# Kernel optimization log

Measured on AMD Instinct MI355X. Metric: run time of the kernel, lower is better.

The kernel has to match this reference:

```python
import jax, jax.numpy as jnp
import numpy as np


def setup_inputs() -> dict:
    key = jax.random.key(0)
    k1, k2, k3 = jax.random.split(key, 3)
    B, Lx, Ly, D = 8, 2048, 2048, 512  # D = 2*hidden_size
    x = jax.random.normal(k1, (B, Lx, D), dtype=jnp.float32)
    y = jax.random.normal(k2, (B, Ly, D), dtype=jnp.float32)
    # torch nn.Linear weight: [out_features, in_features], applied as x @ W.T
    Wb = jax.random.normal(k3, (D, D), dtype=jnp.float32) * (1.0 / np.sqrt(D))
    return {"x": x, "y": y, "Wb": Wb}


def reference(x, y, Wb):
    # _s1 = Wb(x).transpose(2,1): project x then transpose -> scores s_jt = y @ (x Wb^T)^T
    xw = jnp.einsum('bxd,ed->bxe', x, Wb)          # [B, Lx, D], equals x @ Wb.T
    sjt = jnp.einsum('byd,bxd->byx', y, xw)        # [B, Ly, Lx]
    ait = jax.nn.softmax(sjt, axis=-1)             # softmax over Lx
    qtb = jnp.einsum('byx,bxd->byd', ait, x)       # [B, Ly, D]
    return qtb
```

## Files before the change

kernel.cpp:

```cpp
#include <hip/hip_runtime.h>
#include <hip/hip_bf16.h>
#include <math.h>

#define D_DIM 512
#define LX 2048
#define LY 2048
#define NB 8

typedef float f32x4 __attribute__((ext_vector_type(4)));
typedef __bf16 bf16x8 __attribute__((ext_vector_type(8)));

__device__ __forceinline__ unsigned short f2bf_rn(float f) {
    unsigned u = __float_as_uint(f);
    unsigned r = (u + 0x7fffu + ((u >> 16) & 1u)) >> 16;
    return (unsigned short)r;
}
__device__ __forceinline__ float bf2f(unsigned short h) {
    return __uint_as_float(((unsigned)h) << 16);
}
__device__ __forceinline__ void async16(void* lds, const void* g) {
    __builtin_amdgcn_global_load_lds(
        (const __attribute__((address_space(1))) void*)g,
        (__attribute__((address_space(3))) void*)lds, 16, 0, 0);
}
__device__ __forceinline__ bf16x8 ldfrag(const char* p) {
    return *(const bf16x8*)p;
}

__global__ __launch_bounds__(256) void prep_k(
    const float* __restrict__ x, const float* __restrict__ y,
    const float* __restrict__ Wb,
    unsigned short* __restrict__ xfh, unsigned short* __restrict__ xfl,
    unsigned short* __restrict__ yfh, unsigned short* __restrict__ yfl,
    unsigned short* __restrict__ wfh, unsigned short* __restrict__ wfl,
    unsigned short* __restrict__ xtf)
{
    __shared__ unsigned short T2[64][72];
    const int blk = blockIdx.x, tid = threadIdx.x;

    if (blk < 8320) {
        const float* src; unsigned short *dh, *dl; int base;
        if (blk < 4096)      { src = x;  dh = xfh; dl = xfl; base = blk; }
        else if (blk < 8192) { src = y;  dh = yfh; dl = yfl; base = blk - 4096; }
        else                 { src = Wb; dh = wfh; dl = wfl; base = blk - 8192; }
        int fbid = base * 4 + (tid >> 6);
        int lane = tid & 63;
        int r16 = fbid >> 4, k32 = fbid & 15;
        int row = r16 * 16 + (lane & 15);
        int col = k32 * 32 + (lane >> 4) * 8;
        const float* s = src + (size_t)row * D_DIM + col;
        float4 v0 = *(const float4*)s;
        float4 v1 = *(const float4*)(s + 4);
        float vv[8] = {v0.x, v0.y, v0.z, v0.w, v1.x, v1.y, v1.z, v1.w};
        unsigned hh[4], ll[4];
        #pragma unroll
        for (int k = 0; k < 4; ++k) {
            unsigned short ha = f2bf_rn(vv[2*k]),   hb = f2bf_rn(vv[2*k+1]);
            unsigned short la = f2bf_rn(vv[2*k]   - bf2f(ha));
            unsigned short lb = f2bf_rn(vv[2*k+1] - bf2f(hb));
            hh[k] = (unsigned)ha | ((unsigned)hb << 16);
            ll[k] = (unsigned)la | ((unsigned)lb << 16);
        }
        size_t off = (size_t)fbid * 512 + lane * 8;
        *(uint4*)(dh + off) = make_uint4(hh[0], hh[1], hh[2], hh[3]);
        *(uint4*)(dl + off) = make_uint4(ll[0], ll[1], ll[2], ll[3]);
    } else {
        int idx = blk - 8320;
        int ct = idx & 31, dt = (idx >> 5) & 7, b = idx >> 8;
        const float* xb = x + (size_t)b * LX * D_DIM;
        int rc = tid >> 4;
        int d4 = (tid & 15) * 4;
        #pragma unroll
        for (int i = 0; i < 4; ++i) {
            int cl = rc + i * 16;
            float4 v = *(const float4*)(xb + (size_t)(ct * 64 + cl) * D_DIM + dt * 64 + d4);
            T2[d4 + 0][cl] = f2bf_rn(v.x);
            T2[d4 + 1][cl] = f2bf_rn(v.y);
            T2[d4 + 2][cl] = f2bf_rn(v.z);
            T2[d4 + 3][cl] = f2bf_rn(v.w);
        }
        __syncthreads();
        #pragma unroll
        for (int si = 0; si < 2; ++si) {
            int s = tid + si * 256;
            int fb = s >> 6, lane = s & 63;
            int dd16l = fb >> 1, c32l = fb & 1;
            int ddl = dd16l * 16 + (lane & 15);
            int cl  = c32l * 32 + (lane >> 4) * 8;
            uint4 v = *(const uint4*)&T2[ddl][cl];
            size_t off = ((size_t)((b * 32 + dt * 4 + dd16l) * 64 + (ct * 2 + c32l)) * 64 + lane) * 8;
            *(uint4*)(xtf + off) = v;
        }
    }
}

__global__ __launch_bounds__(256, 2) void xw_mfma_k(
    const unsigned short* __restrict__ xfh, const unsigned short* __restrict__ xfl,
    const unsigned short* __restrict__ wfh, const unsigned short* __restrict__ wfl,
    unsigned short* __restrict__ xwfh, unsigned short* __restrict__ xwfl)
{
    __shared__ char smem[49152];
    const int tid = threadIdx.x, lane = tid & 63, w = tid >> 6;
    const int Mt = blockIdx.x, Nt = blockIdx.y;

    f32x4 acc[2][4];
    #pragma unroll
    for (int m = 0; m < 2; ++m)
        #pragma unroll
        for (int n = 0; n < 4; ++n) acc[m][n] = (f32x4){0.f, 0.f, 0.f, 0.f};

    auto stage = [&](int kc, int buf) {
        char* sb = smem + buf * 24576;
        #pragma unroll
        for (int i = 0; i < 4; ++i) {
            int s = w + 4 * i;
            int c16l = s >> 1, h = s & 1;
            size_t fb = ((size_t)(Mt * 8 + c16l)) * 16 + kc;
            const unsigned short* src = (h ? xfl : xfh) + fb * 512 + lane * 8;
            async16(sb + h * 8192 + c16l * 1024 + lane * 16, src);
        }
        #pragma unroll
        for (int i = 0; i < 2; ++i) {
            int s = w + 4 * i;
            int n16l = s >> 1, h = s & 1;
            size_t fb = ((size_t)(Nt * 4 + n16l)) * 16 + kc;
            const unsigned short* src = (h ? wfl : wfh) + fb * 512 + lane * 8;
            async16(sb + 16384 + h * 4096 + n16l * 1024 + lane * 16, src);
        }
    };

    stage(0, 0);
    __syncthreads();
    for (int kc = 0; kc < 16; ++kc) {
        if (kc < 15) stage(kc + 1, (kc + 1) & 1);
        char* sb = smem + (kc & 1) * 24576;
        bf16x8 ah[2], al[2], bh[4], bl[4];
        #pragma unroll
        for (int m = 0; m < 2; ++m) {
            int c16l = w * 2 + m;
            ah[m] = ldfrag(sb + c16l * 1024 + lane * 16);
            al[m] = ldfrag(sb + 8192 + c16l * 1024 + lane * 16);
        }
        #pragma unroll
        for (int n = 0; n < 4; ++n) {
            bh[n] = ldfrag(sb + 16384 + n * 1024 + lane * 16);
            bl[n] = ldfrag(sb + 20480 + n * 1024 + lane * 16);
        }
        #pragma unroll
        for (int m = 0; m < 2; ++m)
            #pragma unroll
            for (int n = 0; n < 4; ++n) {
                acc[m][n] = __builtin_amdgcn_mfma_f32_16x16x32_bf16(ah[m], bh[n], acc[m][n], 0, 0, 0);
                acc[m][n] = __builtin_amdgcn_mfma_f32_16x16x32_bf16(ah[m], bl[n], acc[m][n], 0, 0, 0);
                acc[m][n] = __builtin_amdgcn_mfma_f32_16x16x32_bf16(al[m], bh[n], acc[m][n], 0, 0, 0);
            }
        __syncthreads();
    }

    float* E = (float*)smem;
    const int q = lane >> 4, c15 = lane & 15;
    #pragma unroll
    for (int m = 0; m < 2; ++m)
        #pragma unroll
        for (int n = 0; n < 4; ++n)
            #pragma unroll
            for (int r = 0; r < 4; ++r)
                E[(w * 32 + m * 16 + q * 4 + r) * 68 + n * 16 + c15] = acc[m][n][r];
    __syncthreads();
    #pragma unroll
    for (int i = 0; i < 4; ++i) {
        int s = tid + i * 256;
        int c16l = s >> 7, e32l = (s >> 6) & 1, lp = s & 63;
        int row = c16l * 16 + (lp & 15), col = e32l * 32 + (lp >> 4) * 8;
        const float* sp = E + row * 68 + col;
        unsigned hh[4], ll[4];
        #pragma unroll
        for (int k = 0; k < 4; ++k) {
            float a = sp[2 * k], bq = sp[2 * k + 1];
            unsigned short ha = f2bf_rn(a), hb = f2bf_rn(bq);
            unsigned short la = f2bf_rn(a - bf2f(ha)), lb = f2bf_rn(bq - bf2f(hb));
            hh[k] = (unsigned)ha | ((unsigned)hb << 16);
            ll[k] = (unsigned)la | ((unsigned)lb << 16);
        }
        size_t fb = (size_t)(Mt * 8 + c16l) * 16 + (Nt * 2 + e32l);
        *(uint4*)(xwfh + fb * 512 + lp * 8) = make_uint4(hh[0], hh[1], hh[2], hh[3]);
        *(uint4*)(xwfl + fb * 512 + lp * 8) = make_uint4(ll[0], ll[1], ll[2], ll[3]);
    }
}

#define SBUF_STRIDE 20480

__global__ __launch_bounds__(256, 2) void flash3_k(
    const unsigned short* __restrict__ yfh, const unsigned short* __restrict__ yfl,
    const unsigned short* __restrict__ xwfh, const unsigned short* __restrict__ xwfl,
    const unsigned short* __restrict__ xtf, float* __restrict__ out)
{
    __shared__ char smem[74752];
    const int tid = threadIdx.x, lane = tid & 63, w = tid >> 6;
    const int jt = blockIdx.x, b = blockIdx.y;
    const int q = lane >> 4, c15 = lane & 15;
    unsigned short* Pf = (unsigned short*)(smem + 65536);
    float* red_max = (float*)(smem + 73728);
    float* red_sum = (float*)(smem + 74240);

    f32x4 o[2][8];
    #pragma unroll
    for (int m = 0; m < 2; ++m)
        #pragma unroll
        for (int n = 0; n < 8; ++n) o[m][n] = (f32x4){0.f, 0.f, 0.f, 0.f};
    float m_run[2][4], l_run[2][4];
    #pragma unroll
    for (int m = 0; m < 2; ++m)
        #pragma unroll
        for (int r = 0; r < 4; ++r) { m_run[m][r] = -INFINITY; l_run[m][r] = 0.f; }

    auto stage_s = [&](int xt, int kc, int buf) {
        char* sb = smem + buf * SBUF_STRIDE;
        #pragma unroll
        for (int i = 0; i < 4; ++i) {
            int s = w + 4 * i;
            int c16l = s >> 1, h = s & 1;
            size_t fb = ((size_t)(b * 128 + xt * 8 + c16l)) * 16 + kc;
            const unsigned short* src = (h ? xwfl : xwfh) + fb * 512 + lane * 8;
            async16(sb + h * 8192 + c16l * 1024 + lane * 16, src);
        }
        {
            int j16l = w & 1, h = w >> 1;
            size_t fb = ((size_t)(b * 128 + jt * 2 + j16l)) * 16 + kc;
            const unsigned short* src = (h ? yfl : yfh) + fb * 512 + lane * 8;
            async16(sb + 16384 + h * 2048 + j16l * 1024 + lane * 16, src);
        }
    };
    auto stage_x = [&](int xt, int cc, int buf) {
        char* xb = smem + buf * 32768;
        #pragma unroll
        for (int i = 0; i < 8; ++i) {
            int dd16 = w + 4 * i;
            size_t off = (((size_t)(b * 32 + dd16)) * 64 + (xt * 4 + cc)) * 512 + lane * 8;
            async16(xb + dd16 * 1024 + lane * 16, xtf + off);
        }
    };

    for (int xt = 0; xt < 16; ++xt) {
        f32x4 sa[2][2];
        #pragma unroll
        for (int m = 0; m < 2; ++m)
            #pragma unroll
            for (int n = 0; n < 2; ++n) sa[m][n] = (f32x4){0.f, 0.f, 0.f, 0.f};

        stage_s(xt, 0, 0);
        __syncthreads();
        for (int kc = 0; kc < 16; ++kc) {
            if (kc < 15) stage_s(xt, kc + 1, (kc + 1) & 1);
            char* sb = smem + (kc & 1) * SBUF_STRIDE;
            bf16x8 ah[2], al[2];
            ah[0] = ldfrag(sb + 16384 + lane * 16);
            ah[1] = ldfrag(sb + 17408 + lane * 16);
            al[0] = ldfrag(sb + 18432 + lane * 16);
            al[1] = ldfrag(sb + 19456 + lane * 16);
            #pragma unroll
            for (int n = 0; n < 2; ++n) {
                int c16l = w * 2 + n;
                bf16x8 bh = ldfrag(sb + c16l * 1024 + lane * 16);
                bf16x8 bl = ldfrag(sb + 8192 + c16l * 1024 + lane * 16);
                #pragma unroll
                for (int m = 0; m < 2; ++m) {
                    sa[m][n] = __builtin_amdgcn_mfma_f32_16x16x32_bf16(ah[m], bh, sa[m][n], 0, 0, 0);
                    sa[m][n] = __builtin_amdgcn_mfma_f32_16x16x32_bf16(ah[m], bl, sa[m][n], 0, 0, 0);
                    sa[m][n] = __builtin_amdgcn_mfma_f32_16x16x32_bf16(al[m], bh, sa[m][n], 0, 0, 0);
                }
            }
            __syncthreads();
        }

        float pmax[2][4];
        #pragma unroll
        for (int m = 0; m < 2; ++m)
            #pragma unroll
            for (int r = 0; r < 4; ++r) pmax[m][r] = fmaxf(sa[m][0][r], sa[m][1][r]);
        #pragma unroll
        for (int d = 1; d < 16; d <<= 1)
            #pragma unroll
            for (int m = 0; m < 2; ++m)
                #pragma unroll
                for (int r = 0; r < 4; ++r)
                    pmax[m][r] = fmaxf(pmax[m][r], __shfl_xor(pmax[m][r], d, 64));
        if (c15 == 0) {
            #pragma unroll
            for (int m = 0; m < 2; ++m)
                #pragma unroll
                for (int r = 0; r < 4; ++r)
                    red_max[w * 32 + m * 16 + q * 4 + r] = pmax[m][r];
        }
        __syncthreads();
        float mnew[2][4], alpha[2][4];
        #pragma unroll
        for (int m = 0; m < 2; ++m)
            #pragma unroll
            for (int r = 0; r < 4; ++r) {
                int j = m * 16 + q * 4 + r;
                float t = fmaxf(fmaxf(red_max[j], red_max[32 + j]),
                                fmaxf(red_max[64 + j], red_max[96 + j]));
                float mn = fmaxf(m_run[m][r], t);
                mnew[m][r] = mn;
                alpha[m][r] = __expf(m_run[m][r] - mn);
                m_run[m][r] = mn;
            }
        float psum[2][4] = {};
        #pragma unroll
        for (int m = 0; m < 2; ++m)
            #pragma unroll
            for (int n = 0; n < 2; ++n)
                #pragma unroll
                for (int r = 0; r < 4; ++r) {
                    float p = __expf(sa[m][n][r] - mnew[m][r]);
                    sa[m][n][r] = p;
                    psum[m][r] += (n == 0) ? p - psum[m][r] * 0.f : p;
                }
        #pragma unroll
        for (int d = 1; d < 16; d <<= 1)
            #pragma unroll
            for (int m = 0; m < 2; ++m)
                #pragma unroll
                for (int r = 0; r < 4; ++r)
                    psum[m][r] += __shfl_xor(psum[m][r], d, 64);
        if (c15 == 0) {
            #pragma unroll
            for (int m = 0; m < 2; ++m)
                #pragma unroll
                for (int r = 0; r < 4; ++r)
                    red_sum[w * 32 + m * 16 + q * 4 + r] = psum[m][r];
        }
        #pragma unroll
        for (int m = 0; m < 2; ++m)
            #pragma unroll
            for (int n = 0; n < 2; ++n)
                #pragma unroll
                for (int r = 0; r < 4; ++r) {
                    int cl = n * 16 + c15;
                    int lp = (q * 4 + r) + 16 * (cl >> 3);
                    Pf[((m * 4 + w) * 64 + lp) * 8 + (cl & 7)] = f2bf_rn(sa[m][n][r]);
                }
        __syncthreads();
        #pragma unroll
        for (int m = 0; m < 2; ++m)
            #pragma unroll
            for (int r = 0; r < 4; ++r) {
                int j = m * 16 + q * 4 + r;
                float ts = red_sum[j] + red_sum[32 + j] + red_sum[64 + j] + red_sum[96 + j];
                l_run[m][r] = l_run[m][r] * alpha[m][r] + ts;
            }
        #pragma unroll
        for (int m = 0; m < 2; ++m)
            #pragma unroll
            for (int n = 0; n < 8; ++n)
                #pragma unroll
                for (int r = 0; r < 4; ++r) o[m][n][r] *= alpha[m][r];

        stage_x(xt, 0, 0);
        __syncthreads();
        for (int cc = 0; cc < 4; ++cc) {
            if (cc < 3) stage_x(xt, cc + 1, (cc + 1) & 1);
            char* xb = smem + (cc & 1) * 32768;
            bf16x8 pa0 = ldfrag((const char*)Pf + ((0 * 4 + cc) * 64 + lane) * 16);
            bf16x8 pa1 = ldfrag((const char*)Pf + ((1 * 4 + cc) * 64 + lane) * 16);
            #pragma unroll
            for (int n = 0; n < 8; ++n) {
                bf16x8 xv = ldfrag(xb + (w * 8 + n) * 1024 + lane * 16);
                o[0][n] = __builtin_amdgcn_mfma_f32_16x16x32_bf16(pa0, xv, o[0][n], 0, 0, 0);
                o[1][n] = __builtin_amdgcn_mfma_f32_16x16x32_bf16(pa1, xv, o[1][n], 0, 0, 0);
            }
            __syncthreads();
        }
    }

    #pragma unroll
    for (int m = 0; m < 2; ++m)
        #pragma unroll
        for (int r = 0; r < 4; ++r) {
            float inv = 1.0f / l_run[m][r];
            int j = jt * 32 + m * 16 + q * 4 + r;
            #pragma unroll
            for (int n = 0; n < 8; ++n) {
                int dd = w * 128 + n * 16 + c15;
                out[((size_t)(b * 2048 + j)) * 512 + dd] = o[m][n][r] * inv;
            }
        }
}

__global__ __launch_bounds__(256) void xw_gemm_fb(
    const float* __restrict__ x, const float* __restrict__ Wb, float* __restrict__ xw)
{
    __shared__ float As[16][68];
    __shared__ float Bs[16][68];
    const int tid = threadIdx.x;
    const int bm = blockIdx.x * 64, bn = blockIdx.y * 64;
    const int tm = (tid & 15) * 4, tn = (tid >> 4) * 4;
    const int lrow = tid >> 2, lk = (tid & 3) * 4;
    const float* ag = x  + (size_t)(bm + lrow) * D_DIM + lk;
    const float* bg = Wb + (size_t)(bn + lrow) * D_DIM + lk;
    float acc[4][4] = {};
    for (int kt = 0; kt < D_DIM; kt += 16) {
        const float4 av = *(const float4*)(ag + kt);
        const float4 bv = *(const float4*)(bg + kt);
        __syncthreads();
        As[lk+0][lrow] = av.x; As[lk+1][lrow] = av.y; As[lk+2][lrow] = av.z; As[lk+3][lrow] = av.w;
        Bs[lk+0][lrow] = bv.x; Bs[lk+1][lrow] = bv.y; Bs[lk+2][lrow] = bv.z; Bs[lk+3][lrow] = bv.w;
        __syncthreads();
        #pragma unroll
        for (int k = 0; k < 16; ++k) {
            const float4 a = *(const float4*)&As[k][tm];
            const float4 bq = *(const float4*)&Bs[k][tn];
            const float* ap = (const float*)&a;
            const float* bp = (const float*)&bq;
            #pragma unroll
            for (int i = 0; i < 4; ++i)
                #pragma unroll
                for (int jj = 0; jj < 4; ++jj)
                    acc[i][jj] = fmaf(ap[i], bp[jj], acc[i][jj]);
        }
    }
    #pragma unroll
    for (int i = 0; i < 4; ++i)
        *(float4*)&xw[(size_t)(bm + tm + i) * D_DIM + bn + tn] =
            make_float4(acc[i][0], acc[i][1], acc[i][2], acc[i][3]);
}

__global__ __launch_bounds__(256) void flash_fb(
    const float* __restrict__ x, const float* __restrict__ y,
    const float* __restrict__ xw, float* __restrict__ out)
{
    __shared__ float Yl[16][516];
    __shared__ float XWl[64][68];
    __shared__ float Pl[16][68];
    __shared__ float Xl[8][512];
    const int tid = threadIdx.x, b = blockIdx.y, jtb = blockIdx.x;
    const int j = tid >> 4, tc = tid & 15, c0 = tc * 4;
    {
        const float* yg = y + (size_t)(b * LY + jtb * 16 + j) * D_DIM;
        #pragma unroll
        for (int ii = 0; ii < 8; ++ii)
            *(float4*)&Yl[j][tc * 4 + 64 * ii] = *(const float4*)(yg + tc * 4 + 64 * ii);
    }
    float4 o[8];
    #pragma unroll
    for (int ii = 0; ii < 8; ++ii) o[ii] = make_float4(0.f, 0.f, 0.f, 0.f);
    float m = -INFINITY, l = 0.f;
    const size_t xbase = (size_t)b * LX * D_DIM;
    for (int xtt = 0; xtt < LX / 64; ++xtt) {
        float sa[4] = {0.f, 0.f, 0.f, 0.f};
        for (int kcc = 0; kcc < D_DIM; kcc += 64) {
            const int sc = tid >> 2, skq = (tid & 3) * 4;
            const float* xwg = xw + xbase + (size_t)(xtt * 64 + sc) * D_DIM + kcc + skq;
            const float4 t0 = *(const float4*)(xwg + 0);
            const float4 t1 = *(const float4*)(xwg + 16);
            const float4 t2 = *(const float4*)(xwg + 32);
            const float4 t3 = *(const float4*)(xwg + 48);
            __syncthreads();
            XWl[skq+ 0][sc]=t0.x; XWl[skq+ 1][sc]=t0.y; XWl[skq+ 2][sc]=t0.z; XWl[skq+ 3][sc]=t0.w;
            XWl[skq+16][sc]=t1.x; XWl[skq+17][sc]=t1.y; XWl[skq+18][sc]=t1.z; XWl[skq+19][sc]=t1.w;
            XWl[skq+32][sc]=t2.x; XWl[skq+33][sc]=t2.y; XWl[skq+34][sc]=t2.z; XWl[skq+35][sc]=t2.w;
            XWl[skq+48][sc]=t3.x; XWl[skq+49][sc]=t3.y; XWl[skq+50][sc]=t3.z; XWl[skq+51][sc]=t3.w;
            __syncthreads();
            #pragma unroll
            for (int k4 = 0; k4 < 16; ++k4) {
                const float4 yv = *(const float4*)&Yl[j][kcc + k4 * 4];
                const float* yp = (const float*)&yv;
                #pragma unroll
                for (int ss = 0; ss < 4; ++ss) {
                    const float4 xv = *(const float4*)&XWl[k4 * 4 + ss][c0];
                    sa[0] = fmaf(yp[ss], xv.x, sa[0]);
                    sa[1] = fmaf(yp[ss], xv.y, sa[1]);
                    sa[2] = fmaf(yp[ss], xv.z, sa[2]);
                    sa[3] = fmaf(yp[ss], xv.w, sa[3]);
                }
            }
        }
        float tmax = fmaxf(fmaxf(sa[0], sa[1]), fmaxf(sa[2], sa[3]));
        #pragma unroll
        for (int ww = 1; ww < 16; ww <<= 1) tmax = fmaxf(tmax, __shfl_xor(tmax, ww, 64));
        const float mnew = fmaxf(m, tmax);
        const float scale = __expf(m - mnew);
        const float p0 = __expf(sa[0] - mnew), p1 = __expf(sa[1] - mnew);
        const float p2 = __expf(sa[2] - mnew), p3 = __expf(sa[3] - mnew);
        float ts = p0 + p1 + p2 + p3;
        #pragma unroll
        for (int ww = 1; ww < 16; ww <<= 1) ts += __shfl_xor(ts, ww, 64);
        l = l * scale + ts; m = mnew;
        #pragma unroll
        for (int ii = 0; ii < 8; ++ii) {
            o[ii].x *= scale; o[ii].y *= scale; o[ii].z *= scale; o[ii].w *= scale;
        }
        *(float4*)&Pl[j][c0] = make_float4(p0, p1, p2, p3);
        for (int ccc = 0; ccc < 8; ++ccc) {
            const int xr = tid >> 5, xq = (tid & 31) * 4;
            const float* xg = x + xbase + (size_t)(xtt * 64 + ccc * 8 + xr) * D_DIM + xq;
            const float4 x0 = *(const float4*)(xg + 0);
            const float4 x1 = *(const float4*)(xg + 128);
            const float4 x2 = *(const float4*)(xg + 256);
            const float4 x3 = *(const float4*)(xg + 384);
            __syncthreads();
            *(float4*)&Xl[xr][xq +   0] = x0; *(float4*)&Xl[xr][xq + 128] = x1;
            *(float4*)&Xl[xr][xq + 256] = x2; *(float4*)&Xl[xr][xq + 384] = x3;
            __syncthreads();
            #pragma unroll
            for (int c = 0; c < 8; ++c) {
                const float pv = Pl[j][ccc * 8 + c];
                #pragma unroll
                for (int ii = 0; ii < 8; ++ii) {
                    const float4 xv = *(const float4*)&Xl[c][tc * 4 + 64 * ii];
                    o[ii].x = fmaf(pv, xv.x, o[ii].x); o[ii].y = fmaf(pv, xv.y, o[ii].y);
                    o[ii].z = fmaf(pv, xv.z, o[ii].z); o[ii].w = fmaf(pv, xv.w, o[ii].w);
                }
            }
        }
    }
    const float inv = 1.0f / l;
    float* og = out + (size_t)(b * LY + jtb * 16 + j) * D_DIM;
    #pragma unroll
    for (int ii = 0; ii < 8; ++ii) {
        float4 v = o[ii];
        v.x *= inv; v.y *= inv; v.z *= inv; v.w *= inv;
        *(float4*)(og + tc * 4 + 64 * ii) = v;
    }
}

extern "C" void kernel_launch(void* const* d_in, const int* in_sizes, int n_in,
                              void* d_out, int out_size, void* d_ws, size_t ws_size,
                              hipStream_t stream)
{
    const float* x  = (const float*)d_in[0];
    const float* y  = (const float*)d_in[1];
    const float* Wb = (const float*)d_in[2];
    float* out = (float*)d_out;

    const size_t OFF_XFH = 0,         OFF_XFL = 16777216;
    const size_t OFF_YFH = 33554432,  OFF_YFL = 50331648;
    const size_t OFF_XTF = 67108864;
    const size_t OFF_XWH = 83886080,  OFF_XWL = 100663296;
    const size_t OFF_WFH = 117440512, OFF_WFL = 117964800;
    const size_t NEEDED  = 118489088;

    if (ws_size >= NEEDED) {
        char* ws = (char*)d_ws;
        unsigned short* xfh = (unsigned short*)(ws + OFF_XFH);
        unsigned short* xfl = (unsigned short*)(ws + OFF_XFL);
        unsigned short* yfh = (unsigned short*)(ws + OFF_YFH);
        unsigned short* yfl = (unsigned short*)(ws + OFF_YFL);
        unsigned short* xtf = (unsigned short*)(ws + OFF_XTF);
        unsigned short* xwfh = (unsigned short*)(ws + OFF_XWH);
        unsigned short* xwfl = (unsigned short*)(ws + OFF_XWL);
        unsigned short* wfh = (unsigned short*)(ws + OFF_WFH);
        unsigned short* wfl = (unsigned short*)(ws + OFF_WFL);

        prep_k<<<10368, 256, 0, stream>>>(x, y, Wb, xfh, xfl, yfh, yfl, wfh, wfl, xtf);
        dim3 g1(128, 8);
        xw_mfma_k<<<g1, 256, 0, stream>>>(xfh, xfl, wfh, wfl, xwfh, xwfl);
        dim3 g2(64, 8);
        flash3_k<<<g2, 256, 0, stream>>>(yfh, yfl, xwfh, xwfl, xtf, out);
    } else {
        float* xw = (float*)d_ws;
        dim3 g1(NB * LX / 64, D_DIM / 64);
        xw_gemm_fb<<<g1, 256, 0, stream>>>(x, Wb, xw);
        dim3 g2(LY / 16, NB);
        flash_fb<<<g2, 256, 0, stream>>>(x, y, xw, out);
    }
}
```

Before: 383.6 us.

## Double flash tile to 64 rows x 256 cols with 512-thread blocks

The attention kernel now uses 8 waves per block, split into 2 row halves by 4 column groups. Each block covers 64 query rows and 256 x positions per outer step, so there are half as many outer iterations and blocks. This is meant to raise operand reuse in shared memory and cut global reloads of the x and xW tiles per query row. It also issues the first x-tile prefetch before the softmax math to overlap that load with the exponentials. The cost is more LDS (about 114 KB) and twice as many score accumulators per wave, which may limit the kernel to one block per CU.

```diff
diff --git a/kernel.cpp b/kernel.cpp
--- a/kernel.cpp
+++ b/kernel.cpp
@@ -188,20 +188,22 @@
     }
 }
 
-#define SBUF_STRIDE 20480
-
-__global__ __launch_bounds__(256, 2) void flash3_k(
+#define SBUF 40960
+
+__global__ __launch_bounds__(512, 2) void flash4_k(
     const unsigned short* __restrict__ yfh, const unsigned short* __restrict__ yfl,
     const unsigned short* __restrict__ xwfh, const unsigned short* __restrict__ xwfl,
     const unsigned short* __restrict__ xtf, float* __restrict__ out)
 {
-    __shared__ char smem[74752];
+    __shared__ char smem[116736];
     const int tid = threadIdx.x, lane = tid & 63, w = tid >> 6;
     const int jt = blockIdx.x, b = blockIdx.y;
     const int q = lane >> 4, c15 = lane & 15;
-    unsigned short* Pf = (unsigned short*)(smem + 65536);
-    float* red_max = (float*)(smem + 73728);
-    float* red_sum = (float*)(smem + 74240);
+    const int jh = w >> 2;
+    const int cw = w & 3;
+    unsigned short* Pf = (unsigned short*)(smem + 81920);
+    float* red_max = (float*)(smem + 114688);
+    float* red_sum = (float*)(smem + 115712);
 
     f32x4 o[2][8];
     #pragma unroll
@@ -215,54 +217,55 @@
         for (int r = 0; r < 4; ++r) { m_run[m][r] = -INFINITY; l_run[m][r] = 0.f; }
 
     auto stage_s = [&](int xt, int kc, int buf) {
-        char* sb = smem + buf * SBUF_STRIDE;
+        char* sb = smem + buf * SBUF;
         #pragma unroll
         for (int i = 0; i < 4; ++i) {
-            int s = w + 4 * i;
+            int s = w + 8 * i;
             int c16l = s >> 1, h = s & 1;
-            size_t fb = ((size_t)(b * 128 + xt * 8 + c16l)) * 16 + kc;
+            size_t fb = ((size_t)(b * 128 + xt * 16 + c16l)) * 16 + kc;
             const unsigned short* src = (h ? xwfl : xwfh) + fb * 512 + lane * 8;
-            async16(sb + h * 8192 + c16l * 1024 + lane * 16, src);
+            async16(sb + h * 16384 + c16l * 1024 + lane * 16, src);
         }
         {
-            int j16l = w & 1, h = w >> 1;
-            size_t fb = ((size_t)(b * 128 + jt * 2 + j16l)) * 16 + kc;
+            int j16l = w & 3, h = w >> 2;
+            size_t fb = ((size_t)(b * 128 + jt * 4 + j16l)) * 16 + kc;
             const unsigned short* src = (h ? yfl : yfh) + fb * 512 + lane * 8;
-            async16(sb + 16384 + h * 2048 + j16l * 1024 + lane * 16, src);
+            async16(sb + 32768 + h * 4096 + j16l * 1024 + lane * 16, src);
         }
     };
     auto stage_x = [&](int xt, int cc, int buf) {
-        char* xb = smem + buf * 32768;
-        #pragma unroll
-        for (int i = 0; i < 8; ++i) {
-            int dd16 = w + 4 * i;
-            size_t off = (((size_t)(b * 32 + dd16)) * 64 + (xt * 4 + cc)) * 512 + lane * 8;
+        char* xb = smem + buf * SBUF;
+        #pragma unroll
+        for (int i = 0; i < 4; ++i) {
+            int dd16 = w + 8 * i;
+            size_t off = (((size_t)(b * 32 + dd16)) * 64 + (xt * 8 + cc)) * 512 + lane * 8;
             async16(xb + dd16 * 1024 + lane * 16, xtf + off);
         }
     };
 
-    for (int xt = 0; xt < 16; ++xt) {
-        f32x4 sa[2][2];
-        #pragma unroll
-        for (int m = 0; m < 2; ++m)
-            #pragma unroll
-            for (int n = 0; n < 2; ++n) sa[m][n] = (f32x4){0.f, 0.f, 0.f, 0.f};
+    for (int xt = 0; xt < 8; ++xt) {
+        f32x4 sa[2][4];
+        #pragma unroll
+        for (int m = 0; m < 2; ++m)
+            #pragma unroll
+            for (int n = 0; n < 4; ++n) sa[m][n] = (f32x4){0.f, 0.f, 0.f, 0.f};
 
         stage_s(xt, 0, 0);
         __syncthreads();
         for (int kc = 0; kc < 16; ++kc) {
             if (kc < 15) stage_s(xt, kc + 1, (kc + 1) & 1);
-            char* sb = smem + (kc & 1) * SBUF_STRIDE;
+            char* sb = smem + (kc & 1) * SBUF;
             bf16x8 ah[2], al[2];
-            ah[0] = ldfrag(sb + 16384 + lane * 16);
-            ah[1] = ldfrag(sb + 17408 + lane * 16);
-            al[0] = ldfrag(sb + 18432 + lane * 16);
-            al[1] = ldfrag(sb + 19456 + lane * 16);
-            #pragma unroll
-            for (int n = 0; n < 2; ++n) {
-                int c16l = w * 2 + n;
+            #pragma unroll
+            for (int m = 0; m < 2; ++m) {
+                ah[m] = ldfrag(sb + 32768 + (jh * 2 + m) * 1024 + lane * 16);
+                al[m] = ldfrag(sb + 36864 + (jh * 2 + m) * 1024 + lane * 16);
+            }
+            #pragma unroll
+            for (int n = 0; n < 4; ++n) {
+                int c16l = cw * 4 + n;
                 bf16x8 bh = ldfrag(sb + c16l * 1024 + lane * 16);
-                bf16x8 bl = ldfrag(sb + 8192 + c16l * 1024 + lane * 16);
+                bf16x8 bl = ldfrag(sb + 16384 + c16l * 1024 + lane * 16);
                 #pragma unroll
                 for (int m = 0; m < 2; ++m) {
                     sa[m][n] = __builtin_amdgcn_mfma_f32_16x16x32_bf16(ah[m], bh, sa[m][n], 0, 0, 0);
@@ -277,7 +280,9 @@
         #pragma unroll
         for (int m = 0; m < 2; ++m)
             #pragma unroll
-            for (int r = 0; r < 4; ++r) pmax[m][r] = fmaxf(sa[m][0][r], sa[m][1][r]);
+            for (int r = 0; r < 4; ++r)
+                pmax[m][r] = fmaxf(fmaxf(sa[m][0][r], sa[m][1][r]),
+                                   fmaxf(sa[m][2][r], sa[m][3][r]));
         #pragma unroll
         for (int d = 1; d < 16; d <<= 1)
             #pragma unroll
@@ -290,17 +295,18 @@
             for (int m = 0; m < 2; ++m)
                 #pragma unroll
                 for (int r = 0; r < 4; ++r)
-                    red_max[w * 32 + m * 16 + q * 4 + r] = pmax[m][r];
-        }
-        __syncthreads();
+                    red_max[cw * 64 + jh * 32 + m * 16 + q * 4 + r] = pmax[m][r];
+        }
+        __syncthreads();
+        stage_x(xt, 0, 0);
         float mnew[2][4], alpha[2][4];
         #pragma unroll
         for (int m = 0; m < 2; ++m)
             #pragma unroll
             for (int r = 0; r < 4; ++r) {
-                int j = m * 16 + q * 4 + r;
-                float t = fmaxf(fmaxf(red_max[j], red_max[32 + j]),
-                                fmaxf(red_max[64 + j], red_max[96 + j]));
+                int j = jh * 32 + m * 16 + q * 4 + r;
+                float t = fmaxf(fmaxf(red_max[j], red_max[64 + j]),
+                                fmaxf(red_max[128 + j], red_max[192 + j]));
                 float mn = fmaxf(m_run[m][r], t);
                 mnew[m][r] = mn;
                 alpha[m][r] = __expf(m_run[m][r] - mn);
@@ -310,12 +316,12 @@
         #pragma unroll
         for (int m = 0; m < 2; ++m)
             #pragma unroll
-            for (int n = 0; n < 2; ++n)
+            for (int n = 0; n < 4; ++n)
                 #pragma unroll
                 for (int r = 0; r < 4; ++r) {
                     float p = __expf(sa[m][n][r] - mnew[m][r]);
                     sa[m][n][r] = p;
-                    psum[m][r] += (n == 0) ? p - psum[m][r] * 0.f : p;
+                    psum[m][r] += p;
                 }
         #pragma unroll
         for (int d = 1; d < 16; d <<= 1)
@@ -329,25 +335,25 @@
             for (int m = 0; m < 2; ++m)
                 #pragma unroll
                 for (int r = 0; r < 4; ++r)
-                    red_sum[w * 32 + m * 16 + q * 4 + r] = psum[m][r];
-        }
-        #pragma unroll
-        for (int m = 0; m < 2; ++m)
-            #pragma unroll
-            for (int n = 0; n < 2; ++n)
+                    red_sum[cw * 64 + jh * 32 + m * 16 + q * 4 + r] = psum[m][r];
+        }
+        #pragma unroll
+        for (int m = 0; m < 2; ++m)
+            #pragma unroll
+            for (int n = 0; n < 4; ++n)
                 #pragma unroll
                 for (int r = 0; r < 4; ++r) {
-                    int cl = n * 16 + c15;
-                    int lp = (q * 4 + r) + 16 * (cl >> 3);
-                    Pf[((m * 4 + w) * 64 + lp) * 8 + (cl & 7)] = f2bf_rn(sa[m][n][r]);
+                    int blkP = (jh * 2 + m) * 8 + cw * 2 + (n >> 1);
+                    int lp = (q * 4 + r) + 16 * ((n & 1) * 2 + (c15 >> 3));
+                    Pf[(blkP * 64 + lp) * 8 + (c15 & 7)] = f2bf_rn(sa[m][n][r]);
                 }
         __syncthreads();
         #pragma unroll
         for (int m = 0; m < 2; ++m)
             #pragma unroll
             for (int r = 0; r < 4; ++r) {
-                int j = m * 16 + q * 4 + r;
-                float ts = red_sum[j] + red_sum[32 + j] + red_sum[64 + j] + red_sum[96 + j];
+                int j = jh * 32 + m * 16 + q * 4 + r;
+                float ts = red_sum[j] + red_sum[64 + j] + red_sum[128 + j] + red_sum[192 + j];
                 l_run[m][r] = l_run[m][r] * alpha[m][r] + ts;
             }
         #pragma unroll
@@ -357,16 +363,14 @@
                 #pragma unroll
                 for (int r = 0; r < 4; ++r) o[m][n][r] *= alpha[m][r];
 
-        stage_x(xt, 0, 0);
-        __syncthreads();
-        for (int cc = 0; cc < 4; ++cc) {
-            if (cc < 3) stage_x(xt, cc + 1, (cc + 1) & 1);
-            char* xb = smem + (cc & 1) * 32768;
-            bf16x8 pa0 = ldfrag((const char*)Pf + ((0 * 4 + cc) * 64 + lane) * 16);
-            bf16x8 pa1 = ldfrag((const char*)Pf + ((1 * 4 + cc) * 64 + lane) * 16);
+        for (int cc = 0; cc < 8; ++cc) {
+            if (cc < 7) stage_x(xt, cc + 1, (cc + 1) & 1);
+            char* xb = smem + (cc & 1) * SBUF;
+            bf16x8 pa0 = ldfrag((const char*)Pf + (((jh * 2 + 0) * 8 + cc) * 64 + lane) * 16);
+            bf16x8 pa1 = ldfrag((const char*)Pf + (((jh * 2 + 1) * 8 + cc) * 64 + lane) * 16);
             #pragma unroll
             for (int n = 0; n < 8; ++n) {
-                bf16x8 xv = ldfrag(xb + (w * 8 + n) * 1024 + lane * 16);
+                bf16x8 xv = ldfrag(xb + (cw * 8 + n) * 1024 + lane * 16);
                 o[0][n] = __builtin_amdgcn_mfma_f32_16x16x32_bf16(pa0, xv, o[0][n], 0, 0, 0);
                 o[1][n] = __builtin_amdgcn_mfma_f32_16x16x32_bf16(pa1, xv, o[1][n], 0, 0, 0);
             }
@@ -379,10 +383,10 @@
         #pragma unroll
         for (int r = 0; r < 4; ++r) {
             float inv = 1.0f / l_run[m][r];
-            int j = jt * 32 + m * 16 + q * 4 + r;
+            int j = jt * 64 + jh * 32 + m * 16 + q * 4 + r;
             #pragma unroll
             for (int n = 0; n < 8; ++n) {
-                int dd = w * 128 + n * 16 + c15;
+                int dd = cw * 128 + n * 16 + c15;
                 out[((size_t)(b * 2048 + j)) * 512 + dd] = o[m][n][r] * inv;
             }
         }
@@ -556,8 +560,8 @@
         prep_k<<<10368, 256, 0, stream>>>(x, y, Wb, xfh, xfl, yfh, yfl, wfh, wfl, xtf);
         dim3 g1(128, 8);
         xw_mfma_k<<<g1, 256, 0, stream>>>(xfh, xfl, wfh, wfl, xwfh, xwfl);
-        dim3 g2(64, 8);
-        flash3_k<<<g2, 256, 0, stream>>>(yfh, yfl, xwfh, xwfl, xtf, out);
+        dim3 g2(32, 8);
+        flash4_k<<<g2, 512, 0, stream>>>(yfh, yfl, xwfh, xwfl, xtf, out);
     } else {
         float* xw = (float*)d_ws;
         dim3 g1(NB * LX / 64, D_DIM / 64);
```

New measurement: 328.8 us. 1.17x faster.
